# Kernel tuning notes

Hardware: AMD Instinct MI355X
Metric: run time of the kernel (lower is better)

Reference implementation:

```python
import jax, jax.numpy as jnp
import numpy as np

# SLAYER neuron params (from network.yaml defaults)
THETA = 10.0      # spike threshold
TAU_SR = 10.0     # synaptic (PSP) time constant
TAU_REF = 1.0     # refractory time constant
SCALE_REF = 2.0   # refractory strength (in units of theta)
TAU_RHO = 1.0     # surrogate-gradient width
SCALE_RHO = 1.0   # surrogate-gradient scale
TS = 1.0          # simulation timestep


@jax.custom_vjp
def spike_heaviside(u):
    # SLAYER spike generation: hard threshold in forward
    return (u >= THETA).astype(u.dtype)

def _spk_fwd(u):
    return spike_heaviside(u), u

def _spk_bwd(u, g):
    # SLAYER surrogate: rho(u) = (scaleRho/tauRho) * exp(-|u - theta| / tauRho)
    surr = (SCALE_RHO / TAU_RHO) * jnp.exp(-jnp.abs(u - THETA) / TAU_RHO)
    return (g * surr,)

spike_heaviside.defvjp(_spk_fwd, _spk_bwd)


def psp(x):
    """Temporal post-synaptic-potential filter (exponential synapse kernel).
    x: (B, T, F) -> (B, T, F);  p[t] = decay * p[t-1] + x[t]."""
    decay = jnp.exp(jnp.asarray(-TS / TAU_SR, x.dtype))
    def step(p, xt):
        p = decay * p + xt
        return p, p
    p0 = jnp.zeros((x.shape[0], x.shape[2]), x.dtype)
    _, ps = jax.lax.scan(step, p0, jnp.swapaxes(x, 0, 1))  # scan over T
    return jnp.swapaxes(ps, 0, 1)


def spike(u):
    """Thresholded spike generation with refractory feedback.
    u: (B, T, F) membrane input; refractory state subtracts 2*theta after a spike
    and decays with tauRef (SLAYER refractory response)."""
    decay_ref = jnp.exp(jnp.asarray(-TS / TAU_REF, u.dtype))
    def step(r, ut):
        v = ut + r
        s = spike_heaviside(v)
        r = decay_ref * (r - SCALE_REF * THETA * s)
        return r, s
    r0 = jnp.zeros((u.shape[0], u.shape[2]), u.dtype)
    _, ss = jax.lax.scan(step, r0, jnp.swapaxes(u, 0, 1))  # scan over T
    return jnp.swapaxes(ss, 0, 1)


def setup_inputs() -> dict:
    key = jax.random.key(0)
    k1, k2, k3 = jax.random.split(key, 3)
    B, T, F_IN, F_H, F_OUT = 64, 500, 1250, 512, 2
    x = (jax.random.uniform(k1, (B, T, F_IN)) < 0.1).astype(jnp.float32)
    W1 = jax.random.normal(k2, (F_H, F_IN), jnp.float32) * 0.05
    W2 = jax.random.normal(k3, (F_OUT, F_H), jnp.float32) * 0.05
    return {"x": x, "W1": W1, "W2": W2}


def reference(x, W1, W2):
    # layer 1: dense projection per timestep -> PSP filter -> spike
    s1 = spike(psp(jnp.einsum('btf,hf->bth', x, W1)))   # (B, T, 512)
    # layer 2
    out = spike(psp(jnp.einsum('bth,oh->bto', s1, W2))) # (B, T, 2)
    return out
```

## Files before the change

### kernel.cpp

```cpp
#include <hip/hip_runtime.h>
#include <hip/hip_bf16.h>
#include <cstdint>
#include <cstddef>

#define B_N   64
#define T_N   500
#define K_IN  1250
#define N_H   512
#define N_OUT 2
#define M_N   (B_N * T_N)

#define BM 128
#define BN 128
#define BK 32

static_assert(M_N % BM == 0, "M tiling");
static_assert(N_H % BN == 0, "N tiling");

typedef __attribute__((ext_vector_type(8))) short bf16x8;
typedef __attribute__((ext_vector_type(4))) float f32x4;

#define DECAY_SR  0.9048374180359595732f
#define DECAY_REF 0.3678794411714423216f
#define THETA 10.0f

__device__ __forceinline__ short f2bf(float f) {
  union { float f; uint32_t u; } v; v.f = f;
  uint32_t r = v.u + 0x7FFFu + ((v.u >> 16) & 1u);
  return (short)(r >> 16);
}
__device__ __forceinline__ float bf2f(short s) {
  union { uint32_t u; float f; } v;
  v.u = ((uint32_t)(uint16_t)s) << 16;
  return v.f;
}

__global__ __launch_bounds__(256) void gemm1_kernel(const float* __restrict__ X,
                                                    const float* __restrict__ W1,
                                                    float* __restrict__ U1) {
  __shared__ short As[BM][BK];
  __shared__ short Bs[BN][BK];
  const int tid  = threadIdx.x;
  const int bm   = blockIdx.x * BM;
  const int bn   = blockIdx.y * BN;
  const int w    = tid >> 6;
  const int lane = tid & 63;
  const int wr   = w >> 1;
  const int wc   = w & 1;
  const int lrow = lane & 15;
  const int lgrp = lane >> 4;

  f32x4 acc[4][4];
  #pragma unroll
  for (int i = 0; i < 4; ++i)
    #pragma unroll
    for (int j = 0; j < 4; ++j)
      acc[i][j] = (f32x4){0.f, 0.f, 0.f, 0.f};

  for (int k0 = 0; k0 < K_IN; k0 += BK) {
    #pragma unroll
    for (int rr = 0; rr < 4; ++rr) {
      int j   = rr * 256 + tid;
      int row = j >> 3;
      int kq  = (j & 7) * 4;
      int gk  = k0 + kq;
      const float* srcA = X  + (size_t)(bm + row) * K_IN + gk;
      const float* srcB = W1 + (size_t)(bn + row) * K_IN + gk;
      float a0, a1, a2, a3, b0, b1, b2, b3;
      if (gk + 3 < K_IN) {
        float2 x0 = *(const float2*)srcA;
        float2 x1 = *(const float2*)(srcA + 2);
        float2 y0 = *(const float2*)srcB;
        float2 y1 = *(const float2*)(srcB + 2);
        a0 = x0.x; a1 = x0.y; a2 = x1.x; a3 = x1.y;
        b0 = y0.x; b1 = y0.y; b2 = y1.x; b3 = y1.y;
      } else {
        a0 = (gk + 0 < K_IN) ? srcA[0] : 0.f;
        a1 = (gk + 1 < K_IN) ? srcA[1] : 0.f;
        a2 = (gk + 2 < K_IN) ? srcA[2] : 0.f;
        a3 = (gk + 3 < K_IN) ? srcA[3] : 0.f;
        b0 = (gk + 0 < K_IN) ? srcB[0] : 0.f;
        b1 = (gk + 1 < K_IN) ? srcB[1] : 0.f;
        b2 = (gk + 2 < K_IN) ? srcB[2] : 0.f;
        b3 = (gk + 3 < K_IN) ? srcB[3] : 0.f;
      }
      short4 ha; ha.x = f2bf(a0); ha.y = f2bf(a1); ha.z = f2bf(a2); ha.w = f2bf(a3);
      short4 hb; hb.x = f2bf(b0); hb.y = f2bf(b1); hb.z = f2bf(b2); hb.w = f2bf(b3);
      *(short4*)&As[row][kq] = ha;
      *(short4*)&Bs[row][kq] = hb;
    }
    __syncthreads();

    bf16x8 af[4], bfv[4];
    #pragma unroll
    for (int i = 0; i < 4; ++i) {
      af[i]  = *(const bf16x8*)&As[wr * 64 + i * 16 + lrow][lgrp * 8];
      bfv[i] = *(const bf16x8*)&Bs[wc * 64 + i * 16 + lrow][lgrp * 8];
    }
    #pragma unroll
    for (int i = 0; i < 4; ++i)
      #pragma unroll
      for (int j = 0; j < 4; ++j)
        acc[i][j] = __builtin_amdgcn_mfma_f32_16x16x32_bf16(af[i], bfv[j], acc[i][j], 0, 0, 0);
    __syncthreads();
  }

  #pragma unroll
  for (int i = 0; i < 4; ++i) {
    int rowb = bm + wr * 64 + i * 16 + lgrp * 4;
    #pragma unroll
    for (int j = 0; j < 4; ++j) {
      int col = bn + wc * 64 + j * 16 + lrow;
      #pragma unroll
      for (int r = 0; r < 4; ++r)
        U1[(size_t)(rowb + r) * N_H + col] = acc[i][j][r];
    }
  }
}

__global__ __launch_bounds__(256) void scan1_kernel(const float* __restrict__ U1,
                                                    short* __restrict__ S1) {
  int idx = blockIdx.x * 256 + threadIdx.x;
  int b = idx >> 9, h = idx & 511;
  const float* u = U1 + (size_t)b * T_N * N_H + h;
  short*       s = S1 + (size_t)b * T_N * N_H + h;
  float p = 0.f, r = 0.f;
  for (int t0 = 0; t0 < T_N; t0 += 10) {
    float buf[10];
    #pragma unroll
    for (int j = 0; j < 10; ++j) buf[j] = u[(size_t)(t0 + j) * N_H];
    #pragma unroll
    for (int j = 0; j < 10; ++j) {
      p = DECAY_SR * p + buf[j];
      float v = p + r;
      float sp = (v >= THETA) ? 1.f : 0.f;
      r = DECAY_REF * (r - 2.f * THETA * sp);
      s[(size_t)(t0 + j) * N_H] = (sp > 0.f) ? (short)0x3F80 : (short)0;
    }
  }
}

__global__ __launch_bounds__(256) void gemm2_kernel(const short* __restrict__ S1,
                                                    const float* __restrict__ W2,
                                                    float* __restrict__ U2) {
  int m    = blockIdx.x * 4 + (threadIdx.x >> 6);
  int lane = threadIdx.x & 63;
  const bf16x8 sv = *(const bf16x8*)&S1[(size_t)m * N_H + lane * 8];
  float a0 = 0.f, a1 = 0.f;
  #pragma unroll
  for (int j = 0; j < 8; ++j) {
    float sj = bf2f(sv[j]);
    a0 += sj * W2[lane * 8 + j];
    a1 += sj * W2[N_H + lane * 8 + j];
  }
  #pragma unroll
  for (int off = 32; off >= 1; off >>= 1) {
    a0 += __shfl_down(a0, off);
    a1 += __shfl_down(a1, off);
  }
  if (lane == 0) {
    U2[(size_t)m * 2]     = a0;
    U2[(size_t)m * 2 + 1] = a1;
  }
}

__global__ __launch_bounds__(128) void scan2_kernel(const float* __restrict__ U2,
                                                    float* __restrict__ OUT) {
  __shared__ float lu[T_N * 2];
  __shared__ float ls[T_N * 2];
  int b = blockIdx.x;
  const float* src = U2 + (size_t)b * T_N * 2;
  for (int i = threadIdx.x; i < T_N * 2; i += 128) lu[i] = src[i];
  __syncthreads();
  if (threadIdx.x < 2) {
    int o = threadIdx.x;
    float p = 0.f, r = 0.f;
    for (int t = 0; t < T_N; ++t) {
      p = DECAY_SR * p + lu[t * 2 + o];
      float v = p + r;
      float sp = (v >= THETA) ? 1.f : 0.f;
      r = DECAY_REF * (r - 2.f * THETA * sp);
      ls[t * 2 + o] = sp;
    }
  }
  __syncthreads();
  float* dst = OUT + (size_t)b * T_N * 2;
  for (int i = threadIdx.x; i < T_N * 2; i += 128) dst[i] = ls[i];
}

extern "C" void kernel_launch(void* const* d_in, const int* in_sizes, int n_in,
                              void* d_out, int out_size, void* d_ws, size_t ws_size,
                              hipStream_t stream) {
  const float* X  = (const float*)d_in[0];
  const float* W1 = (const float*)d_in[1];
  const float* W2 = (const float*)d_in[2];
  float* OUT = (float*)d_out;

  char* ws = (char*)d_ws;
  float* U1 = (float*)ws;
  short* S1 = (short*)(ws + (size_t)M_N * N_H * 4);
  float* U2 = (float*)(ws + (size_t)M_N * N_H * 6);

  gemm1_kernel<<<dim3(M_N / BM, N_H / BN), 256, 0, stream>>>(X, W1, U1);
  scan1_kernel<<<dim3((B_N * N_H) / 256), 256, 0, stream>>>(U1, S1);
  gemm2_kernel<<<dim3(M_N / 4), 256, 0, stream>>>(S1, W2, U2);
  scan2_kernel<<<dim3(B_N), 128, 0, stream>>>(U2, OUT);
}
```

Baseline: 404.8 us.

## Pre-convert W1 to bf16, widen GEMM1 tile to full N, store U1 as bf16

Adds a pre-pass that converts W1 to padded bf16 once. GEMM1 is restructured so each 1024-thread block covers all 512 hidden columns, which means X is read and converted only once instead of once per N tile. W1 tiles are loaded straight into LDS via global_load_lds with an XOR swizzle to avoid bank conflicts. The U1 intermediate is stored as bf16 to halve the write and scan read traffic. This risks threshold flips from rounding the membrane input to bf16, plus lower occupancy from the large block.

```diff
diff --git a/kernel.cpp b/kernel.cpp
--- a/kernel.cpp
+++ b/kernel.cpp
@@ -6,16 +6,12 @@
 #define B_N   64
 #define T_N   500
 #define K_IN  1250
+#define KP    1280
 #define N_H   512
-#define N_OUT 2
 #define M_N   (B_N * T_N)
 
 #define BM 128
-#define BN 128
 #define BK 32
-
-static_assert(M_N % BM == 0, "M tiling");
-static_assert(N_H % BN == 0, "N tiling");
 
 typedef __attribute__((ext_vector_type(8))) short bf16x8;
 typedef __attribute__((ext_vector_type(4))) float f32x4;
@@ -29,109 +25,124 @@
   uint32_t r = v.u + 0x7FFFu + ((v.u >> 16) & 1u);
   return (short)(r >> 16);
 }
-__device__ __forceinline__ float bf2f(short s) {
+__device__ __forceinline__ float bf2f(unsigned short s) {
   union { uint32_t u; float f; } v;
-  v.u = ((uint32_t)(uint16_t)s) << 16;
+  v.u = ((uint32_t)s) << 16;
   return v.f;
 }
 
-__global__ __launch_bounds__(256) void gemm1_kernel(const float* __restrict__ X,
-                                                    const float* __restrict__ W1,
-                                                    float* __restrict__ U1) {
-  __shared__ short As[BM][BK];
-  __shared__ short Bs[BN][BK];
+__global__ __launch_bounds__(256) void w1cvt_kernel(const float* __restrict__ W1,
+                                                    short* __restrict__ W1b) {
+  int k = blockIdx.x * 256 + threadIdx.x;
+  int n = blockIdx.y;
+  float v = (k < K_IN) ? W1[(size_t)n * K_IN + k] : 0.f;
+  W1b[(size_t)n * KP + k] = f2bf(v);
+}
+
+__global__ __launch_bounds__(1024) void gemm1_kernel(const float* __restrict__ X,
+                                                     const short* __restrict__ W1b,
+                                                     unsigned short* __restrict__ U1) {
+  __shared__ short As[BM * BK];
+  __shared__ short Bs[N_H * BK];
   const int tid  = threadIdx.x;
   const int bm   = blockIdx.x * BM;
-  const int bn   = blockIdx.y * BN;
   const int w    = tid >> 6;
   const int lane = tid & 63;
-  const int wr   = w >> 1;
-  const int wc   = w & 1;
+  const int wr   = w >> 2;
+  const int wc   = w & 3;
   const int lrow = lane & 15;
   const int lgrp = lane >> 4;
-
-  f32x4 acc[4][4];
-  #pragma unroll
-  for (int i = 0; i < 4; ++i)
-    #pragma unroll
-    for (int j = 0; j < 4; ++j)
+  const int lsw  = lgrp ^ (lrow & 3);
+
+  f32x4 acc[2][8];
+  #pragma unroll
+  for (int i = 0; i < 2; ++i)
+    #pragma unroll
+    for (int j = 0; j < 8; ++j)
       acc[i][j] = (f32x4){0.f, 0.f, 0.f, 0.f};
 
-  for (int k0 = 0; k0 < K_IN; k0 += BK) {
-    #pragma unroll
-    for (int rr = 0; rr < 4; ++rr) {
-      int j   = rr * 256 + tid;
-      int row = j >> 3;
-      int kq  = (j & 7) * 4;
-      int gk  = k0 + kq;
-      const float* srcA = X  + (size_t)(bm + row) * K_IN + gk;
-      const float* srcB = W1 + (size_t)(bn + row) * K_IN + gk;
-      float a0, a1, a2, a3, b0, b1, b2, b3;
+  const int arow  = tid >> 3;
+  const int akq   = (tid & 7) * 4;
+  const int aslot = akq >> 3;
+  const int asub  = akq & 7;
+  const int awofs = arow * BK + ((aslot ^ (arow & 3)) * 8) + asub;
+
+  const int bn0   = w * 32 + (lane >> 2);
+  const int bslot = lane & 3;
+
+  for (int k0 = 0; k0 < KP; k0 += BK) {
+    #pragma unroll
+    for (int c = 0; c < 2; ++c) {
+      int n = bn0 + c * 16;
+      int sslot = bslot ^ (n & 3);
+      const short* src = W1b + (size_t)n * KP + k0 + sslot * 8;
+      short* dst = &Bs[(w * 2 + c) * 512];
+      __builtin_amdgcn_global_load_lds(
+          (const __attribute__((address_space(1))) void*)src,
+          (__attribute__((address_space(3))) void*)dst, 16, 0, 0);
+    }
+    {
+      int gk = k0 + akq;
+      const float* srcA = X + (size_t)(bm + arow) * K_IN + gk;
+      float a0, a1, a2, a3;
       if (gk + 3 < K_IN) {
         float2 x0 = *(const float2*)srcA;
         float2 x1 = *(const float2*)(srcA + 2);
-        float2 y0 = *(const float2*)srcB;
-        float2 y1 = *(const float2*)(srcB + 2);
         a0 = x0.x; a1 = x0.y; a2 = x1.x; a3 = x1.y;
-        b0 = y0.x; b1 = y0.y; b2 = y1.x; b3 = y1.y;
       } else {
         a0 = (gk + 0 < K_IN) ? srcA[0] : 0.f;
         a1 = (gk + 1 < K_IN) ? srcA[1] : 0.f;
         a2 = (gk + 2 < K_IN) ? srcA[2] : 0.f;
         a3 = (gk + 3 < K_IN) ? srcA[3] : 0.f;
-        b0 = (gk + 0 < K_IN) ? srcB[0] : 0.f;
-        b1 = (gk + 1 < K_IN) ? srcB[1] : 0.f;
-        b2 = (gk + 2 < K_IN) ? srcB[2] : 0.f;
-        b3 = (gk + 3 < K_IN) ? srcB[3] : 0.f;
       }
-      short4 ha; ha.x = f2bf(a0); ha.y = f2bf(a1); ha.z = f2bf(a2); ha.w = f2bf(a3);
-      short4 hb; hb.x = f2bf(b0); hb.y = f2bf(b1); hb.z = f2bf(b2); hb.w = f2bf(b3);
-      *(short4*)&As[row][kq] = ha;
-      *(short4*)&Bs[row][kq] = hb;
+      short4 h;
+      h.x = f2bf(a0); h.y = f2bf(a1); h.z = f2bf(a2); h.w = f2bf(a3);
+      *(short4*)&As[awofs] = h;
     }
     __syncthreads();
 
-    bf16x8 af[4], bfv[4];
-    #pragma unroll
-    for (int i = 0; i < 4; ++i) {
-      af[i]  = *(const bf16x8*)&As[wr * 64 + i * 16 + lrow][lgrp * 8];
-      bfv[i] = *(const bf16x8*)&Bs[wc * 64 + i * 16 + lrow][lgrp * 8];
-    }
-    #pragma unroll
-    for (int i = 0; i < 4; ++i)
+    bf16x8 af[2], bfv[8];
+    #pragma unroll
+    for (int i = 0; i < 2; ++i)
+      af[i] = *(const bf16x8*)&As[(wr * 32 + i * 16 + lrow) * BK + lsw * 8];
+    #pragma unroll
+    for (int j = 0; j < 8; ++j)
+      bfv[j] = *(const bf16x8*)&Bs[(wc * 128 + j * 16 + lrow) * BK + lsw * 8];
+    #pragma unroll
+    for (int i = 0; i < 2; ++i)
       #pragma unroll
-      for (int j = 0; j < 4; ++j)
+      for (int j = 0; j < 8; ++j)
         acc[i][j] = __builtin_amdgcn_mfma_f32_16x16x32_bf16(af[i], bfv[j], acc[i][j], 0, 0, 0);
     __syncthreads();
   }
 
   #pragma unroll
-  for (int i = 0; i < 4; ++i) {
-    int rowb = bm + wr * 64 + i * 16 + lgrp * 4;
-    #pragma unroll
-    for (int j = 0; j < 4; ++j) {
-      int col = bn + wc * 64 + j * 16 + lrow;
+  for (int i = 0; i < 2; ++i) {
+    int row0 = bm + wr * 32 + i * 16 + lgrp * 4;
+    #pragma unroll
+    for (int j = 0; j < 8; ++j) {
+      int col = wc * 128 + j * 16 + lrow;
       #pragma unroll
       for (int r = 0; r < 4; ++r)
-        U1[(size_t)(rowb + r) * N_H + col] = acc[i][j][r];
-    }
-  }
-}
-
-__global__ __launch_bounds__(256) void scan1_kernel(const float* __restrict__ U1,
+        U1[(size_t)(row0 + r) * N_H + col] = (unsigned short)f2bf(acc[i][j][r]);
+    }
+  }
+}
+
+__global__ __launch_bounds__(256) void scan1_kernel(const unsigned short* __restrict__ U1,
                                                     short* __restrict__ S1) {
   int idx = blockIdx.x * 256 + threadIdx.x;
   int b = idx >> 9, h = idx & 511;
-  const float* u = U1 + (size_t)b * T_N * N_H + h;
-  short*       s = S1 + (size_t)b * T_N * N_H + h;
+  const unsigned short* u = U1 + (size_t)b * T_N * N_H + h;
+  short*                s = S1 + (size_t)b * T_N * N_H + h;
   float p = 0.f, r = 0.f;
   for (int t0 = 0; t0 < T_N; t0 += 10) {
-    float buf[10];
-    #pragma unroll
-    for (int j = 0; j < 10; ++j) buf[j] = u[(size_t)(t0 + j) * N_H];
+    unsigned short raw[10];
+    #pragma unroll
+    for (int j = 0; j < 10; ++j) raw[j] = u[(size_t)(t0 + j) * N_H];
     #pragma unroll
     for (int j = 0; j < 10; ++j) {
-      p = DECAY_SR * p + buf[j];
+      p = DECAY_SR * p + bf2f(raw[j]);
       float v = p + r;
       float sp = (v >= THETA) ? 1.f : 0.f;
       r = DECAY_REF * (r - 2.f * THETA * sp);
@@ -149,7 +160,7 @@
   float a0 = 0.f, a1 = 0.f;
   #pragma unroll
   for (int j = 0; j < 8; ++j) {
-    float sj = bf2f(sv[j]);
+    float sj = bf2f((unsigned short)sv[j]);
     a0 += sj * W2[lane * 8 + j];
     a1 += sj * W2[N_H + lane * 8 + j];
   }
@@ -197,11 +208,13 @@
   float* OUT = (float*)d_out;
 
   char* ws = (char*)d_ws;
-  float* U1 = (float*)ws;
-  short* S1 = (short*)(ws + (size_t)M_N * N_H * 4);
-  float* U2 = (float*)(ws + (size_t)M_N * N_H * 6);
-
-  gemm1_kernel<<<dim3(M_N / BM, N_H / BN), 256, 0, stream>>>(X, W1, U1);
+  short*          W1b = (short*)ws;
+  unsigned short* U1  = (unsigned short*)(ws + 1310720);
+  short*          S1  = (short*)(ws + 1310720 + 32768000);
+  float*          U2  = (float*)(ws + 1310720 + 2 * 32768000);
+
+  w1cvt_kernel<<<dim3(KP / 256, N_H), 256, 0, stream>>>(W1, W1b);
+  gemm1_kernel<<<dim3(M_N / BM), 1024, 0, stream>>>(X, W1b, U1);
   scan1_kernel<<<dim3((B_N * N_H) / 256), 256, 0, stream>>>(U1, S1);
   gemm2_kernel<<<dim3(M_N / 4), 256, 0, stream>>>(S1, W2, U2);
   scan2_kernel<<<dim3(B_N), 128, 0, stream>>>(U2, OUT);
```

Measured after the change: 357.3 us. 1.13x faster.
